# Kernel tuning notes

Hardware: AMD Instinct MI355X
Metric: run time of the kernel (lower is better)

## Reference

```python
import math
import jax, jax.numpy as jnp
import numpy as np

D_MODEL = 1024
NHEAD = 16
HEAD_DIM = D_MODEL // NHEAD
BATCH = 2
SEQ = 2048


def setup_inputs() -> dict:
    key = jax.random.key(0)
    ks = jax.random.split(key, 8)
    data = jax.random.normal(ks[0], (BATCH, SEQ, D_MODEL), dtype=jnp.float32)
    temporal = jax.random.uniform(ks[1], (BATCH, SEQ), dtype=jnp.float32)
    mask = jnp.zeros((SEQ, SEQ), dtype=jnp.float32)
    s = 1.0 / math.sqrt(D_MODEL)
    Wq = jax.random.normal(ks[2], (D_MODEL, D_MODEL), dtype=jnp.float32) * s
    Wk = jax.random.normal(ks[3], (D_MODEL, D_MODEL), dtype=jnp.float32) * s
    Wv = jax.random.normal(ks[4], (D_MODEL, D_MODEL), dtype=jnp.float32) * s
    bq = jax.random.normal(ks[5], (D_MODEL,), dtype=jnp.float32) * 0.02
    bk = jax.random.normal(ks[6], (D_MODEL,), dtype=jnp.float32) * 0.02
    bv = jax.random.normal(ks[7], (D_MODEL,), dtype=jnp.float32) * 0.02
    return {"data": data, "temporal": temporal, "mask": mask,
            "Wq": Wq, "bq": bq, "Wk": Wk, "bk": bk, "Wv": Wv, "bv": bv}


def _rotate_half_pairs(x):
    # x: [..., s] with s even; pairs (x0,x1) -> (-x1, x0) interleaved
    x2 = x.reshape(x.shape[:-1] + (-1, 2))  # [..., s//2, 2]
    rot = jnp.stack([-x2[..., 1], x2[..., 0]], axis=-1)
    return rot.reshape(x.shape)


def reference(data, temporal, mask, Wq, bq, Wk, bk, Wv, bv):
    B, L, D = data.shape
    H, S = NHEAD, HEAD_DIM
    scale = math.sqrt(S)

    query = (data @ Wq + bq).reshape(B, L, H, S)
    key_ = (data @ Wk + bk).reshape(B, L, H, S)
    value = (data @ Wv + bv).reshape(B, L, H, S)

    # freq = 10000^(-arange(0, S, 2)/S), repeat_interleave(2) -> [S]
    freq = jnp.power(10000.0, -jnp.arange(0, S, 2, dtype=jnp.float32) / S)
    freq = jnp.repeat(freq, 2)
    freqs = temporal[:, :, None] * freq[None, None, :]  # [B, L, S]
    cosine = jnp.cos(freqs)[:, :, None, :]  # [B, L, 1, S]
    sine = jnp.sin(freqs)[:, :, None, :]

    rq = query * cosine + _rotate_half_pairs(query) * sine
    rk = key_ * cosine + _rotate_half_pairs(key_) * sine

    logits = jnp.einsum('bqhs,bkhs->bhqk', rq, rk) / scale
    logits = logits + mask  # mask: [L, L], broadcasts over b,h
    weights = jax.nn.softmax(logits, axis=-1)
    context = jnp.einsum('bhqk,bkhs->bqhs', weights, value)
    return context.reshape(B, L, D)
```

## Files before the change

kernel.cpp:

```cpp
#include <hip/hip_runtime.h>
#include <hip/hip_bf16.h>

#define D_MODEL 1024
#define NHEAD   16
#define HEAD_DIM 64
#define BATCH   2
#define SEQ     2048
#define NTOK    (BATCH*SEQ)

#define FREQ_LOG2 0.20762050593046015f

typedef short  bfrag __attribute__((ext_vector_type(8)));
typedef float  ffrag __attribute__((ext_vector_type(4)));

__device__ inline ushort f2bf(float x) {
    __hip_bfloat16 h = __float2bfloat16(x);
    return __builtin_bit_cast(ushort, h);
}
__device__ inline float bf2f(ushort u) {
    return __builtin_bit_cast(float, (uint)u << 16);
}
__device__ inline void split_bf(float x, ushort& hi, ushort& lo) {
    __hip_bfloat16 h = __float2bfloat16(x);
    hi = __builtin_bit_cast(ushort, h);
    lo = f2bf(x - __bfloat162float(h));
}

__device__ inline void gload16(const ushort* g, ushort* l) {
    __builtin_amdgcn_global_load_lds(
        (const __attribute__((address_space(1))) void*)g,
        (__attribute__((address_space(3))) void*)l, 16, 0, 0);
}

__device__ inline void barrier_lds_only() {
    asm volatile("s_waitcnt lgkmcnt(0)\n\ts_barrier" ::: "memory");
}

__device__ inline void barrier_vm4() {
    asm volatile("s_waitcnt vmcnt(4) lgkmcnt(0)\n\ts_barrier" ::: "memory");
}

__device__ inline void barrier_vm8() {
    asm volatile("s_waitcnt vmcnt(8) lgkmcnt(0)\n\ts_barrier" ::: "memory");
}

__global__ __launch_bounds__(256)
void prep(const float* __restrict__ data, ushort* __restrict__ Ahi,
          ushort* __restrict__ Alo,
          const float* __restrict__ mask, ushort* __restrict__ Mbf,
          int* __restrict__ MZnz,
          const float* __restrict__ Wq, const float* __restrict__ Wk,
          const float* __restrict__ Wv, ushort* __restrict__ WThi,
          const float* __restrict__ temporal, float* __restrict__ cst)
{
    __shared__ float T[64][65];
    __shared__ int bnz;
    const int bid = blockIdx.x, t = threadIdx.x;

    if (bid < 4096) {
        const int i4 = (bid * 256 + t) * 4;
        const float4 v = *(const float4*)(data + i4);
        ushort4 h, l;
        split_bf(v.x, h.x, l.x); split_bf(v.y, h.y, l.y);
        split_bf(v.z, h.z, l.z); split_bf(v.w, h.w, l.w);
        *(ushort4*)(Ahi + i4) = h;
        *(ushort4*)(Alo + i4) = l;
        return;
    }
    if (bid < 8192) {
        const int mi = bid - 4096;
        const int i4 = (mi * 256 + t) * 4;
        const float4 v = *(const float4*)(mask + i4);
        ushort4 h;
        h.x = f2bf(v.x); h.y = f2bf(v.y); h.z = f2bf(v.z); h.w = f2bf(v.w);
        *(ushort4*)(Mbf + i4) = h;
        const int nz = (v.x != 0.f) || (v.y != 0.f) || (v.z != 0.f) || (v.w != 0.f);
        if (t == 0) bnz = 0;
        __syncthreads();
        if (nz) atomicOr(&bnz, 1);
        __syncthreads();
        if (t == 0) MZnz[mi] = bnz;
        return;
    }
    if (bid < 8960) {
        const int id  = bid - 8192;
        const int z   = id >> 8;
        const int rem = id & 255;
        const int k0  = (rem & 15) * 64, n0 = (rem >> 4) * 64;
        const float* W = (z == 0) ? Wq : (z == 1) ? Wk : Wv;
        ushort* thi = WThi + (size_t)z * D_MODEL * D_MODEL;

        #pragma unroll
        for (int i = 0; i < 4; i++) {
            const int f = i * 256 + t, r = f >> 4, c = (f & 15) * 4;
            const float4 v = *(const float4*)(W + (size_t)(k0 + r) * D_MODEL + n0 + c);
            T[r][c] = v.x; T[r][c + 1] = v.y; T[r][c + 2] = v.z; T[r][c + 3] = v.w;
        }
        __syncthreads();
        #pragma unroll
        for (int i = 0; i < 4; i++) {
            const int f = i * 256 + t, nr = f >> 4, kc = (f & 15) * 4;
            ushort4 h;
            h.x = f2bf(T[kc + 0][nr]);
            h.y = f2bf(T[kc + 1][nr]);
            h.z = f2bf(T[kc + 2][nr]);
            h.w = f2bf(T[kc + 3][nr]);
            const size_t o = (size_t)(n0 + nr) * D_MODEL + k0 + kc;
            *(ushort4*)(thi + o) = h;
        }
        return;
    }
    const int id3 = bid - 8960;
    const int m   = id3 * 8 + (t >> 5);
    const int j   = t & 31;
    const float tv = temporal[m];
    const float fr = exp2f(-(float)(2 * j) * FREQ_LOG2);
    float s, c;
    __sincosf(tv * fr, &s, &c);
    *(float2*)(cst + (size_t)m * 64 + 2 * j) = make_float2(c, s);
}

#define BK 32

union GemmSM {
    ushort st[3][2][128 * BK];
    float  c[64 * 132];
};

__global__ __launch_bounds__(256, 3)
void gemm_qkv(const ushort* __restrict__ Ahi, const ushort* __restrict__ Alo,
              const ushort* __restrict__ WThi,
              const float* __restrict__ bq, const float* __restrict__ bk,
              const float* __restrict__ bv, const float* __restrict__ cst,
              const int* __restrict__ MZnz, int* __restrict__ Flag,
              ushort* __restrict__ Qhi, ushort* __restrict__ Qlo,
              ushort* __restrict__ Khi,
              ushort* __restrict__ VT)
{
    __shared__ GemmSM sm;
    __shared__ int flg;
    const int bidl = blockIdx.x;
    const int xcd  = bidl & 7, kk = bidl >> 3;
    const int m0   = (xcd * 4 + (kk & 3)) * 128;
    const int nz   = kk >> 2;
    const int n0   = (nz & 7) * 128;
    const int z    = nz >> 3;

    const int t = threadIdx.x;

    if (bidl == 0) {
        if (t == 0) flg = 0;
        __syncthreads();
        int acc = 0;
        const int4* z4 = (const int4*)MZnz;
        #pragma unroll
        for (int i = 0; i < 4; i++) {
            const int4 v = z4[t * 4 + i];
            acc |= v.x | v.y | v.z | v.w;
        }
        if (acc) atomicOr(&flg, 1);
        __syncthreads();
        if (t == 0) Flag[0] = flg;
    }

    const float* bias = (z == 0) ? bq : (z == 1) ? bk : bv;
    const ushort* Bh = WThi + (size_t)z * D_MODEL * D_MODEL;

    const int w = t >> 6, lane = t & 63;
    const int lane15 = lane & 15, quad8 = (lane >> 4) * 8, quad = lane >> 4;
    const int wm = (w >> 1) * 64, wn = (w & 1) * 64;

    ffrag acc[4][4];
    #pragma unroll
    for (int i = 0; i < 4; i++)
        #pragma unroll
        for (int j = 0; j < 4; j++) acc[i][j] = (ffrag){0.f, 0.f, 0.f, 0.f};

    const int wr = w * 32;
    const int lr = lane >> 2;
    const int lc = (((lane & 3) ^ ((lane >> 3) & 3))) * 8;

    auto stage = [&](int bsel, int k0) {
        #pragma unroll
        for (int ch = 0; ch < 2; ch++) {
            const int rb = wr + ch * 16;
            const ushort* ga = Ahi + (size_t)(m0 + rb + lr) * D_MODEL + k0 + lc;
            const ushort* gb = Bh  + (size_t)(n0 + rb + lr) * D_MODEL + k0 + lc;
            gload16(ga, &sm.st[bsel][0][rb * BK]);
            gload16(gb, &sm.st[bsel][1][rb * BK]);
        }
    };

    bfrag alp0, alp1, alp2, alp3;
    {
        alp0 = *(const bfrag*)(Alo + (size_t)(m0 + wm +  0 + lane15) * D_MODEL + quad8);
        alp1 = *(const bfrag*)(Alo + (size_t)(m0 + wm + 16 + lane15) * D_MODEL + quad8);
        alp2 = *(const bfrag*)(Alo + (size_t)(m0 + wm + 32 + lane15) * D_MODEL + quad8);
        alp3 = *(const bfrag*)(Alo + (size_t)(m0 + wm + 48 + lane15) * D_MODEL + quad8);
    }

    stage(0, 0);
    stage(1, BK);
    barrier_vm4();

    const int rdsw = (quad ^ ((lane15 >> 1) & 3)) * 8;

    int cur = 0;
    for (int i = 0; i < 32; i++) {
        const int k0 = i * BK;
        const int st2 = (cur >= 1) ? cur - 1 : 2;
        stage(st2, k0 + 2 * BK);

        bfrag al0 = alp0, al1 = alp1, al2 = alp2, al3 = alp3;
        {
            const int kn = k0 + BK;
            alp0 = *(const bfrag*)(Alo + (size_t)(m0 + wm +  0 + lane15) * D_MODEL + kn + quad8);
            alp1 = *(const bfrag*)(Alo + (size_t)(m0 + wm + 16 + lane15) * D_MODEL + kn + quad8);
            alp2 = *(const bfrag*)(Alo + (size_t)(m0 + wm + 32 + lane15) * D_MODEL + kn + quad8);
            alp3 = *(const bfrag*)(Alo + (size_t)(m0 + wm + 48 + lane15) * D_MODEL + kn + quad8);
        }

        bfrag ah[4];
        #pragma unroll
        for (int mt = 0; mt < 4; mt++)
            ah[mt] = *(const bfrag*)&sm.st[cur][0][(wm + mt * 16 + lane15) * BK + rdsw];

        #pragma unroll
        for (int nt = 0; nt < 4; nt++) {
            const bfrag bh = *(const bfrag*)&sm.st[cur][1][(wn + nt * 16 + lane15) * BK + rdsw];
            {
                ffrag a = acc[0][nt];
                a = __builtin_amdgcn_mfma_f32_16x16x32_bf16(ah[0], bh, a, 0, 0, 0);
                a = __builtin_amdgcn_mfma_f32_16x16x32_bf16(al0,   bh, a, 0, 0, 0);
                acc[0][nt] = a;
            }
            {
                ffrag a = acc[1][nt];
                a = __builtin_amdgcn_mfma_f32_16x16x32_bf16(ah[1], bh, a, 0, 0, 0);
                a = __builtin_amdgcn_mfma_f32_16x16x32_bf16(al1,   bh, a, 0, 0, 0);
                acc[1][nt] = a;
            }
            {
                ffrag a = acc[2][nt];
                a = __builtin_amdgcn_mfma_f32_16x16x32_bf16(ah[2], bh, a, 0, 0, 0);
                a = __builtin_amdgcn_mfma_f32_16x16x32_bf16(al2,   bh, a, 0, 0, 0);
                acc[2][nt] = a;
            }
            {
                ffrag a = acc[3][nt];
                a = __builtin_amdgcn_mfma_f32_16x16x32_bf16(ah[3], bh, a, 0, 0, 0);
                a = __builtin_amdgcn_mfma_f32_16x16x32_bf16(al3,   bh, a, 0, 0, 0);
                acc[3][nt] = a;
            }
        }
        barrier_vm8();
        cur = (cur == 2) ? 0 : cur + 1;
    }

    float bn[4];
    #pragma unroll
    for (int nt = 0; nt < 4; nt++) bn[nt] = bias[n0 + wn + nt * 16 + lane15];

    const int CST = (z == 2) ? 129 : 132;

    #pragma unroll
    for (int p = 0; p < 2; p++) {
        if (p) __syncthreads();
        if ((w >> 1) == p) {
            #pragma unroll
            for (int mt = 0; mt < 4; mt++)
                #pragma unroll
                for (int nt = 0; nt < 4; nt++)
                    #pragma unroll
                    for (int rr = 0; rr < 4; rr++)
                        sm.c[(mt * 16 + quad * 4 + rr) * CST + wn + nt * 16 + lane15] =
                            acc[mt][nt][rr] + bn[nt];
        }
        __syncthreads();

        if (z < 2) {
            ushort* ohi = (z == 0) ? Qhi : Khi;
            const float sc = (z == 0) ? 0.125f : 1.0f;
            #pragma unroll
            for (int i = 0; i < 8; i++) {
                const int f = i * 256 + t, r = f >> 5, c4 = (f & 31) * 4;
                float4 v = *(float4*)&sm.c[r * 132 + c4];
                const int m = m0 + p * 64 + r;
                const float4 cs4 = *(const float4*)(cst + (size_t)m * 64 + (c4 & 63));
                const float c0 = cs4.x, s0 = cs4.y, c1v = cs4.z, s1 = cs4.w;
                const float y0 = (v.x * c0 - v.y * s0) * sc;
                const float y1 = (v.y * c0 + v.x * s0) * sc;
                const float y2 = (v.z * c1v - v.w * s1) * sc;
                const float y3 = (v.w * c1v + v.z * s1) * sc;
                ushort4 h, l;
                split_bf(y0, h.x, l.x); split_bf(y1, h.y, l.y);
                split_bf(y2, h.z, l.z); split_bf(y3, h.w, l.w);
                const size_t o = (size_t)m * D_MODEL + n0 + c4;
                *(ushort4*)(ohi + o) = h;
                if (z == 0) *(ushort4*)(Qlo + o) = l;
            }
        } else {
            const int bb = m0 >> 11;
            #pragma unroll
            for (int i = 0; i < 4; i++) {
                const int cid = i * 256 + t, col = cid >> 3, tg = (cid & 7) * 8;
                ushort u8[8];
                #pragma unroll
                for (int j = 0; j < 8; j++) u8[j] = f2bf(sm.c[(tg + j) * 129 + col]);
                const int ncol = n0 + col, hh = ncol >> 6, d = ncol & 63;
                const size_t dst = ((size_t)(bb * NHEAD + hh) * HEAD_DIM + d) * SEQ +
                                   (m0 & (SEQ - 1)) + p * 64 + tg;
                *(int4*)(VT + dst) = *(int4*)u8;
            }
        }
    }
}

__global__ __launch_bounds__(256, 2)
void attn_mfma(const ushort* __restrict__ Qhi, const ushort* __restrict__ Qlo,
               const ushort* __restrict__ Khi,
               const ushort* __restrict__ VT,  const ushort* __restrict__ maskbf,
               const int* __restrict__ Flag,
               float* __restrict__ out)
{
    __shared__ ushort lsK[2][64 * 64], lsV[2][64 * 64], lsP[128 * 64];

    const int bid  = blockIdx.x;
    const int bh   = (bid & 7) * 4 + (bid >> 7);
    const int qb   = (bid >> 3) & 15;
    const int b    = bh >> 4, h = bh & 15;
    const int q0   = qb * 128;

    const int t = threadIdx.x, w = t >> 6, lane = t & 63;
    const int lane15 = lane & 15, quad = lane >> 4;
    const size_t tok0 = (size_t)b * SEQ;

    const int mz = Flag[0];

    bfrag qh[2][2], ql[2][2];
    #pragma unroll
    for (int su = 0; su < 2; su++) {
        const size_t qrow = (tok0 + q0 + w * 32 + su * 16 + lane15) * D_MODEL +
                            h * HEAD_DIM;
        #pragma unroll
        for (int ks = 0; ks < 2; ks++) {
            qh[su][ks] = *(const bfrag*)(Qhi + qrow + ks * 32 + quad * 8);
            ql[su][ks] = *(const bfrag*)(Qlo + qrow + ks * 32 + quad * 8);
        }
    }

    ffrag of[2][4];
    float l_i[2][4];
    #pragma unroll
    for (int su = 0; su < 2; su++)
        #pragma unroll
        for (int nt = 0; nt < 4; nt++) {
            of[su][nt] = (ffrag){0.f, 0.f, 0.f, 0.f};
            l_i[su][nt] = 0.f;
        }

    const int r1 = t >> 3,  c1 = (t & 7) * 8;
    const int sw = ((t & 7) ^ (r1 & 7)) * 8;
    const ushort* Kh0 = Khi + tok0 * D_MODEL + h * HEAD_DIM;
    const ushort* Vt0 = VT + (size_t)(b * NHEAD + h) * HEAD_DIM * SEQ;

    int4 pk0 = *(const int4*)(Kh0 + (size_t)r1 * D_MODEL + c1);
    int4 pk1 = *(const int4*)(Kh0 + (size_t)(32 + r1) * D_MODEL + c1);
    int4 pv0 = *(const int4*)(Vt0 + (size_t)r1 * SEQ + c1);
    int4 pv1 = *(const int4*)(Vt0 + (size_t)(32 + r1) * SEQ + c1);

    *(int4*)&lsK[0][r1 * 64 + sw]        = pk0;
    *(int4*)&lsK[0][(32 + r1) * 64 + sw] = pk1;
    *(int4*)&lsV[0][r1 * 64 + sw]        = pv0;
    *(int4*)&lsV[0][(32 + r1) * 64 + sw] = pv1;

    pk0 = *(const int4*)(Kh0 + (size_t)(64 + r1) * D_MODEL + c1);
    pk1 = *(const int4*)(Kh0 + (size_t)(96 + r1) * D_MODEL + c1);
    pv0 = *(const int4*)(Vt0 + (size_t)r1 * SEQ + 64 + c1);
    pv1 = *(const int4*)(Vt0 + (size_t)(32 + r1) * SEQ + 64 + c1);
    barrier_lds_only();

    const ushort* mrow0 = maskbf + (size_t)(q0 + w * 32 + quad * 4) * SEQ;
    const ushort* mrow1 = maskbf + (size_t)(q0 + w * 32 + 16 + quad * 4) * SEQ;

    const int krd  = lane15 & 7;
    const int keyr = (((lane15 >> 2) & 3) << 1) | (lane15 & 1);

    int cur = 0;
    for (int kt = 0; kt < SEQ; kt += 64) {
        if (kt + 64 < SEQ) {
            *(int4*)&lsK[cur ^ 1][r1 * 64 + sw]        = pk0;
            *(int4*)&lsK[cur ^ 1][(32 + r1) * 64 + sw] = pk1;
            *(int4*)&lsV[cur ^ 1][r1 * 64 + sw]        = pv0;
            *(int4*)&lsV[cur ^ 1][(32 + r1) * 64 + sw] = pv1;
        }

        float mv0[4][4], mv1[4][4];
        if (mz) {
            #pragma unroll
            for (int nt = 0; nt < 4; nt++)
                #pragma unroll
                for (int rr = 0; rr < 4; rr++) {
                    mv0[nt][rr] = bf2f(mrow0[(size_t)rr * SEQ + kt + nt * 16 + lane15]);
                    mv1[nt][rr] = bf2f(mrow1[(size_t)rr * SEQ + kt + nt * 16 + lane15]);
                }
        }

        const int ktn = (kt + 128 < SEQ) ? kt + 128 : 0;
        pk0 = *(const int4*)(Kh0 + (size_t)(ktn + r1) * D_MODEL + c1);
        pk1 = *(const int4*)(Kh0 + (size_t)(ktn + 32 + r1) * D_MODEL + c1);
        pv0 = *(const int4*)(Vt0 + (size_t)r1 * SEQ + ktn + c1);
        pv1 = *(const int4*)(Vt0 + (size_t)(32 + r1) * SEQ + ktn + c1);

        ffrag s0[4], s1[4];
        __builtin_amdgcn_s_setprio(1);
        #pragma unroll
        for (int nt = 0; nt < 4; nt++) {
            const bfrag kf0 = *(const bfrag*)&lsK[cur][(nt * 16 + lane15) * 64 +
                                                       ((0 + quad) ^ krd) * 8];
            const bfrag kf1 = *(const bfrag*)&lsK[cur][(nt * 16 + lane15) * 64 +
                                                       ((4 + quad) ^ krd) * 8];
            ffrag a0 = (ffrag){0.f, 0.f, 0.f, 0.f};
            ffrag a1 = (ffrag){0.f, 0.f, 0.f, 0.f};
            a0 = __builtin_amdgcn_mfma_f32_16x16x32_bf16(qh[0][0], kf0, a0, 0, 0, 0);
            a0 = __builtin_amdgcn_mfma_f32_16x16x32_bf16(ql[0][0], kf0, a0, 0, 0, 0);
            a0 = __builtin_amdgcn_mfma_f32_16x16x32_bf16(qh[0][1], kf1, a0, 0, 0, 0);
            a0 = __builtin_amdgcn_mfma_f32_16x16x32_bf16(ql[0][1], kf1, a0, 0, 0, 0);
            a1 = __builtin_amdgcn_mfma_f32_16x16x32_bf16(qh[1][0], kf0, a1, 0, 0, 0);
            a1 = __builtin_amdgcn_mfma_f32_16x16x32_bf16(ql[1][0], kf0, a1, 0, 0, 0);
            a1 = __builtin_amdgcn_mfma_f32_16x16x32_bf16(qh[1][1], kf1, a1, 0, 0, 0);
            a1 = __builtin_amdgcn_mfma_f32_16x16x32_bf16(ql[1][1], kf1, a1, 0, 0, 0);
            s0[nt] = a0;
            s1[nt] = a1;
        }
        __builtin_amdgcn_s_setprio(0);

        #pragma unroll
        for (int nt = 0; nt < 4; nt++)
            #pragma unroll
            for (int rr = 0; rr < 4; rr++) {
                const int pchk = (2 * nt + (lane15 >> 3)) ^ ((quad << 1) | (rr & 1));
                float x0 = s0[nt][rr];
                float x1 = s1[nt][rr];
                if (mz) { x0 += mv0[nt][rr]; x1 += mv1[nt][rr]; }
                const float e0 = __expf(x0);
                l_i[0][rr] += e0;
                lsP[(w * 32 + quad * 4 + rr) * 64 + pchk * 8 + (lane15 & 7)] = f2bf(e0);
                const float e1 = __expf(x1);
                l_i[1][rr] += e1;
                lsP[(w * 32 + 16 + quad * 4 + rr) * 64 + pchk * 8 + (lane15 & 7)] = f2bf(e1);
            }

        __builtin_amdgcn_s_setprio(1);
        #pragma unroll
        for (int ks = 0; ks < 2; ks++) {
            const bfrag pf0 = *(const bfrag*)&lsP[(w * 32 + lane15) * 64 +
                                                  ((ks * 4 + quad) ^ keyr) * 8];
            const bfrag pf1 = *(const bfrag*)&lsP[(w * 32 + 16 + lane15) * 64 +
                                                  ((ks * 4 + quad) ^ keyr) * 8];
            #pragma unroll
            for (int nt = 0; nt < 4; nt++) {
                const bfrag vf = *(const bfrag*)&lsV[cur][(nt * 16 + lane15) * 64 +
                                                          ((ks * 4 + quad) ^ krd) * 8];
                of[0][nt] = __builtin_amdgcn_mfma_f32_16x16x32_bf16(pf0, vf, of[0][nt], 0, 0, 0);
                of[1][nt] = __builtin_amdgcn_mfma_f32_16x16x32_bf16(pf1, vf, of[1][nt], 0, 0, 0);
            }
        }
        __builtin_amdgcn_s_setprio(0);

        barrier_lds_only();
        cur ^= 1;
    }

    #pragma unroll
    for (int su = 0; su < 2; su++) {
        float inv[4];
        #pragma unroll
        for (int rr = 0; rr < 4; rr++) {
            float v = l_i[su][rr];
            #pragma unroll
            for (int off = 1; off < 16; off <<= 1) v += __shfl_xor(v, off);
            inv[rr] = 1.0f / v;
        }
        #pragma unroll
        for (int nt = 0; nt < 4; nt++)
            #pragma unroll
            for (int rr = 0; rr < 4; rr++)
                out[(tok0 + q0 + w * 32 + su * 16 + quad * 4 + rr) * D_MODEL +
                    h * HEAD_DIM + nt * 16 + lane15] = of[su][nt][rr] * inv[rr];
    }
}

extern "C" void kernel_launch(void* const* d_in, const int* in_sizes, int n_in,
                              void* d_out, int out_size, void* d_ws, size_t ws_size,
                              hipStream_t stream)
{
    const float* data     = (const float*)d_in[0];
    const float* temporal = (const float*)d_in[1];
    const float* mask     = (const float*)d_in[2];
    const float* Wq = (const float*)d_in[3];
    const float* bq = (const float*)d_in[4];
    const float* Wk = (const float*)d_in[5];
    const float* bk = (const float*)d_in[6];
    const float* Wv = (const float*)d_in[7];
    const float* bv = (const float*)d_in[8];
    float* out = (float*)d_out;

    char* ws = (char*)d_ws;
    const size_t MB = 1024 * 1024;
    ushort* Ahi  = (ushort*)(ws + 0 * MB);
    ushort* Alo  = (ushort*)(ws + 8 * MB);
    ushort* WThi = (ushort*)(ws + 16 * MB);
    int*    MZnz = (int*)   (ws + 22 * MB);
    int*    Flag = (int*)   (ws + 23 * MB);
    float*  cst  = (float*) (ws + 24 * MB);
    ushort* Qhi  = (ushort*)(ws + 28 * MB);
    ushort* Qlo  = (ushort*)(ws + 36 * MB);
    ushort* Khi  = (ushort*)(ws + 44 * MB);
    ushort* VT   = (ushort*)(ws + 60 * MB);
    ushort* Mbf  = (ushort*)(ws + 68 * MB);

    prep<<<dim3(9472), 256, 0, stream>>>(data, Ahi, Alo, mask, Mbf, MZnz,
                                         Wq, Wk, Wv, WThi, temporal, cst);
    gemm_qkv<<<dim3(768), 256, 0, stream>>>(
        Ahi, Alo, WThi, bq, bk, bv, cst, MZnz, Flag,
        Qhi, Qlo, Khi, VT);
    attn_mfma<<<dim3(BATCH * NHEAD * SEQ / 128), 256, 0, stream>>>(
        Qhi, Qlo, Khi, VT, Mbf, Flag, out);
}
```

Measured before the change: 239.7 us.

## Double the K/V tile per pipeline stage to 128 keys with new V swizzle

The attention loop now stages 128 keys of K and V per double-buffered step and processes them as two 64-key halves, so it needs half as many block barriers and prefetch rounds. The V tile layout is widened to 128 columns per row with a new XOR swizzle to avoid LDS bank conflicts. In exchange, LDS usage rises (about 80KB per block with two blocks per CU) and each thread holds more prefetch registers, which could limit occupancy. The lsP tile written in the second half reuses the buffer without an intervening barrier, which relies on per-wave row ownership.

Result: faster. 234.6 us (-2.1%).

```diff
diff --git a/kernel.cpp b/kernel.cpp
--- a/kernel.cpp
+++ b/kernel.cpp
@@ -323,7 +323,7 @@
                const int* __restrict__ Flag,
                float* __restrict__ out)
 {
-    __shared__ ushort lsK[2][64 * 64], lsV[2][64 * 64], lsP[128 * 64];
+    __shared__ ushort lsK[2][128 * 64], lsV[2][64 * 128], lsP[128 * 64];
 
     const int bid  = blockIdx.x;
     const int bh   = (bid & 7) * 4 + (bid >> 7);
@@ -359,25 +359,39 @@
             l_i[su][nt] = 0.f;
         }
 
-    const int r1 = t >> 3,  c1 = (t & 7) * 8;
-    const int sw = ((t & 7) ^ (r1 & 7)) * 8;
+    const int rK  = t >> 3, cK = (t & 7) * 8;
+    const int swK = ((t & 7) ^ (rK & 7)) * 8;
+    const int rV   = t >> 2;
+    const int keyV = ((rV & 3) << 2) | ((rV >> 2) & 3);
     const ushort* Kh0 = Khi + tok0 * D_MODEL + h * HEAD_DIM;
     const ushort* Vt0 = VT + (size_t)(b * NHEAD + h) * HEAD_DIM * SEQ;
 
-    int4 pk0 = *(const int4*)(Kh0 + (size_t)r1 * D_MODEL + c1);
-    int4 pk1 = *(const int4*)(Kh0 + (size_t)(32 + r1) * D_MODEL + c1);
-    int4 pv0 = *(const int4*)(Vt0 + (size_t)r1 * SEQ + c1);
-    int4 pv1 = *(const int4*)(Vt0 + (size_t)(32 + r1) * SEQ + c1);
-
-    *(int4*)&lsK[0][r1 * 64 + sw]        = pk0;
-    *(int4*)&lsK[0][(32 + r1) * 64 + sw] = pk1;
-    *(int4*)&lsV[0][r1 * 64 + sw]        = pv0;
-    *(int4*)&lsV[0][(32 + r1) * 64 + sw] = pv1;
-
-    pk0 = *(const int4*)(Kh0 + (size_t)(64 + r1) * D_MODEL + c1);
-    pk1 = *(const int4*)(Kh0 + (size_t)(96 + r1) * D_MODEL + c1);
-    pv0 = *(const int4*)(Vt0 + (size_t)r1 * SEQ + 64 + c1);
-    pv1 = *(const int4*)(Vt0 + (size_t)(32 + r1) * SEQ + 64 + c1);
+    int4 pk0 = *(const int4*)(Kh0 + (size_t)(rK +  0) * D_MODEL + cK);
+    int4 pk1 = *(const int4*)(Kh0 + (size_t)(rK + 32) * D_MODEL + cK);
+    int4 pk2 = *(const int4*)(Kh0 + (size_t)(rK + 64) * D_MODEL + cK);
+    int4 pk3 = *(const int4*)(Kh0 + (size_t)(rK + 96) * D_MODEL + cK);
+    int4 pv0 = *(const int4*)(Vt0 + (size_t)rV * SEQ + (t & 3) * 8 +  0);
+    int4 pv1 = *(const int4*)(Vt0 + (size_t)rV * SEQ + (t & 3) * 8 + 32);
+    int4 pv2 = *(const int4*)(Vt0 + (size_t)rV * SEQ + (t & 3) * 8 + 64);
+    int4 pv3 = *(const int4*)(Vt0 + (size_t)rV * SEQ + (t & 3) * 8 + 96);
+
+    *(int4*)&lsK[0][(rK +  0) * 64 + swK] = pk0;
+    *(int4*)&lsK[0][(rK + 32) * 64 + swK] = pk1;
+    *(int4*)&lsK[0][(rK + 64) * 64 + swK] = pk2;
+    *(int4*)&lsK[0][(rK + 96) * 64 + swK] = pk3;
+    *(int4*)&lsV[0][rV * 128 + (((t & 3) +  0) ^ keyV) * 8] = pv0;
+    *(int4*)&lsV[0][rV * 128 + (((t & 3) +  4) ^ keyV) * 8] = pv1;
+    *(int4*)&lsV[0][rV * 128 + (((t & 3) +  8) ^ keyV) * 8] = pv2;
+    *(int4*)&lsV[0][rV * 128 + (((t & 3) + 12) ^ keyV) * 8] = pv3;
+
+    pk0 = *(const int4*)(Kh0 + (size_t)(128 + rK +  0) * D_MODEL + cK);
+    pk1 = *(const int4*)(Kh0 + (size_t)(128 + rK + 32) * D_MODEL + cK);
+    pk2 = *(const int4*)(Kh0 + (size_t)(128 + rK + 64) * D_MODEL + cK);
+    pk3 = *(const int4*)(Kh0 + (size_t)(128 + rK + 96) * D_MODEL + cK);
+    pv0 = *(const int4*)(Vt0 + (size_t)rV * SEQ + 128 + (t & 3) * 8 +  0);
+    pv1 = *(const int4*)(Vt0 + (size_t)rV * SEQ + 128 + (t & 3) * 8 + 32);
+    pv2 = *(const int4*)(Vt0 + (size_t)rV * SEQ + 128 + (t & 3) * 8 + 64);
+    pv3 = *(const int4*)(Vt0 + (size_t)rV * SEQ + 128 + (t & 3) * 8 + 96);
     barrier_lds_only();
 
     const ushort* mrow0 = maskbf + (size_t)(q0 + w * 32 + quad * 4) * SEQ;
@@ -385,88 +399,102 @@
 
     const int krd  = lane15 & 7;
     const int keyr = (((lane15 >> 2) & 3) << 1) | (lane15 & 1);
+    const int keyVr = ((lane15 & 3) << 2) | ((lane15 >> 2) & 3);
 
     int cur = 0;
-    for (int kt = 0; kt < SEQ; kt += 64) {
-        if (kt + 64 < SEQ) {
-            *(int4*)&lsK[cur ^ 1][r1 * 64 + sw]        = pk0;
-            *(int4*)&lsK[cur ^ 1][(32 + r1) * 64 + sw] = pk1;
-            *(int4*)&lsV[cur ^ 1][r1 * 64 + sw]        = pv0;
-            *(int4*)&lsV[cur ^ 1][(32 + r1) * 64 + sw] = pv1;
-        }
-
-        float mv0[4][4], mv1[4][4];
-        if (mz) {
+    for (int kt = 0; kt < SEQ; kt += 128) {
+        if (kt + 128 < SEQ) {
+            *(int4*)&lsK[cur ^ 1][(rK +  0) * 64 + swK] = pk0;
+            *(int4*)&lsK[cur ^ 1][(rK + 32) * 64 + swK] = pk1;
+            *(int4*)&lsK[cur ^ 1][(rK + 64) * 64 + swK] = pk2;
+            *(int4*)&lsK[cur ^ 1][(rK + 96) * 64 + swK] = pk3;
+            *(int4*)&lsV[cur ^ 1][rV * 128 + (((t & 3) +  0) ^ keyV) * 8] = pv0;
+            *(int4*)&lsV[cur ^ 1][rV * 128 + (((t & 3) +  4) ^ keyV) * 8] = pv1;
+            *(int4*)&lsV[cur ^ 1][rV * 128 + (((t & 3) +  8) ^ keyV) * 8] = pv2;
+            *(int4*)&lsV[cur ^ 1][rV * 128 + (((t & 3) + 12) ^ keyV) * 8] = pv3;
+        }
+
+        const int ktn = (kt + 256 < SEQ) ? kt + 256 : 0;
+        pk0 = *(const int4*)(Kh0 + (size_t)(ktn + rK +  0) * D_MODEL + cK);
+        pk1 = *(const int4*)(Kh0 + (size_t)(ktn + rK + 32) * D_MODEL + cK);
+        pk2 = *(const int4*)(Kh0 + (size_t)(ktn + rK + 64) * D_MODEL + cK);
+        pk3 = *(const int4*)(Kh0 + (size_t)(ktn + rK + 96) * D_MODEL + cK);
+        pv0 = *(const int4*)(Vt0 + (size_t)rV * SEQ + ktn + (t & 3) * 8 +  0);
+        pv1 = *(const int4*)(Vt0 + (size_t)rV * SEQ + ktn + (t & 3) * 8 + 32);
+        pv2 = *(const int4*)(Vt0 + (size_t)rV * SEQ + ktn + (t & 3) * 8 + 64);
+        pv3 = *(const int4*)(Vt0 + (size_t)rV * SEQ + ktn + (t & 3) * 8 + 96);
+
+        #pragma unroll
+        for (int half = 0; half < 2; half++) {
+            const int kb = kt + half * 64;
+
+            float mv0[4][4], mv1[4][4];
+            if (mz) {
+                #pragma unroll
+                for (int nt = 0; nt < 4; nt++)
+                    #pragma unroll
+                    for (int rr = 0; rr < 4; rr++) {
+                        mv0[nt][rr] = bf2f(mrow0[(size_t)rr * SEQ + kb + nt * 16 + lane15]);
+                        mv1[nt][rr] = bf2f(mrow1[(size_t)rr * SEQ + kb + nt * 16 + lane15]);
+                    }
+            }
+
+            ffrag s0[4], s1[4];
+            __builtin_amdgcn_s_setprio(1);
+            #pragma unroll
+            for (int nt = 0; nt < 4; nt++) {
+                const int krow = half * 64 + nt * 16 + lane15;
+                const bfrag kf0 = *(const bfrag*)&lsK[cur][krow * 64 + ((0 + quad) ^ krd) * 8];
+                const bfrag kf1 = *(const bfrag*)&lsK[cur][krow * 64 + ((4 + quad) ^ krd) * 8];
+                ffrag a0 = (ffrag){0.f, 0.f, 0.f, 0.f};
+                ffrag a1 = (ffrag){0.f, 0.f, 0.f, 0.f};
+                a0 = __builtin_amdgcn_mfma_f32_16x16x32_bf16(qh[0][0], kf0, a0, 0, 0, 0);
+                a0 = __builtin_amdgcn_mfma_f32_16x16x32_bf16(ql[0][0], kf0, a0, 0, 0, 0);
+                a0 = __builtin_amdgcn_mfma_f32_16x16x32_bf16(qh[0][1], kf1, a0, 0, 0, 0);
+                a0 = __builtin_amdgcn_mfma_f32_16x16x32_bf16(ql[0][1], kf1, a0, 0, 0, 0);
+                a1 = __builtin_amdgcn_mfma_f32_16x16x32_bf16(qh[1][0], kf0, a1, 0, 0, 0);
+                a1 = __builtin_amdgcn_mfma_f32_16x16x32_bf16(ql[1][0], kf0, a1, 0, 0, 0);
+                a1 = __builtin_amdgcn_mfma_f32_16x16x32_bf16(qh[1][1], kf1, a1, 0, 0, 0);
+                a1 = __builtin_amdgcn_mfma_f32_16x16x32_bf16(ql[1][1], kf1, a1, 0, 0, 0);
+                s0[nt] = a0;
+                s1[nt] = a1;
+            }
+            __builtin_amdgcn_s_setprio(0);
+
             #pragma unroll
             for (int nt = 0; nt < 4; nt++)
                 #pragma unroll
                 for (int rr = 0; rr < 4; rr++) {
-                    mv0[nt][rr] = bf2f(mrow0[(size_t)rr * SEQ + kt + nt * 16 + lane15]);
-                    mv1[nt][rr] = bf2f(mrow1[(size_t)rr * SEQ + kt + nt * 16 + lane15]);
+                    const int pchk = (2 * nt + (lane15 >> 3)) ^ ((quad << 1) | (rr & 1));
+                    float x0 = s0[nt][rr];
+                    float x1 = s1[nt][rr];
+                    if (mz) { x0 += mv0[nt][rr]; x1 += mv1[nt][rr]; }
+                    const float e0 = __expf(x0);
+                    l_i[0][rr] += e0;
+                    lsP[(w * 32 + quad * 4 + rr) * 64 + pchk * 8 + (lane15 & 7)] = f2bf(e0);
+                    const float e1 = __expf(x1);
+                    l_i[1][rr] += e1;
+                    lsP[(w * 32 + 16 + quad * 4 + rr) * 64 + pchk * 8 + (lane15 & 7)] = f2bf(e1);
                 }
-        }
-
-        const int ktn = (kt + 128 < SEQ) ? kt + 128 : 0;
-        pk0 = *(const int4*)(Kh0 + (size_t)(ktn + r1) * D_MODEL + c1);
-        pk1 = *(const int4*)(Kh0 + (size_t)(ktn + 32 + r1) * D_MODEL + c1);
-        pv0 = *(const int4*)(Vt0 + (size_t)r1 * SEQ + ktn + c1);
-        pv1 = *(const int4*)(Vt0 + (size_t)(32 + r1) * SEQ + ktn + c1);
-
-        ffrag s0[4], s1[4];
-        __builtin_amdgcn_s_setprio(1);
-        #pragma unroll
-        for (int nt = 0; nt < 4; nt++) {
-            const bfrag kf0 = *(const bfrag*)&lsK[cur][(nt * 16 + lane15) * 64 +
-                                                       ((0 + quad) ^ krd) * 8];
-            const bfrag kf1 = *(const bfrag*)&lsK[cur][(nt * 16 + lane15) * 64 +
-                                                       ((4 + quad) ^ krd) * 8];
-            ffrag a0 = (ffrag){0.f, 0.f, 0.f, 0.f};
-            ffrag a1 = (ffrag){0.f, 0.f, 0.f, 0.f};
-            a0 = __builtin_amdgcn_mfma_f32_16x16x32_bf16(qh[0][0], kf0, a0, 0, 0, 0);
-            a0 = __builtin_amdgcn_mfma_f32_16x16x32_bf16(ql[0][0], kf0, a0, 0, 0, 0);
-            a0 = __builtin_amdgcn_mfma_f32_16x16x32_bf16(qh[0][1], kf1, a0, 0, 0, 0);
-            a0 = __builtin_amdgcn_mfma_f32_16x16x32_bf16(ql[0][1], kf1, a0, 0, 0, 0);
-            a1 = __builtin_amdgcn_mfma_f32_16x16x32_bf16(qh[1][0], kf0, a1, 0, 0, 0);
-            a1 = __builtin_amdgcn_mfma_f32_16x16x32_bf16(ql[1][0], kf0, a1, 0, 0, 0);
-            a1 = __builtin_amdgcn_mfma_f32_16x16x32_bf16(qh[1][1], kf1, a1, 0, 0, 0);
-            a1 = __builtin_amdgcn_mfma_f32_16x16x32_bf16(ql[1][1], kf1, a1, 0, 0, 0);
-            s0[nt] = a0;
-            s1[nt] = a1;
-        }
-        __builtin_amdgcn_s_setprio(0);
-
-        #pragma unroll
-        for (int nt = 0; nt < 4; nt++)
-            #pragma unroll
-            for (int rr = 0; rr < 4; rr++) {
-                const int pchk = (2 * nt + (lane15 >> 3)) ^ ((quad << 1) | (rr & 1));
-                float x0 = s0[nt][rr];
-                float x1 = s1[nt][rr];
-                if (mz) { x0 += mv0[nt][rr]; x1 += mv1[nt][rr]; }
-                const float e0 = __expf(x0);
-                l_i[0][rr] += e0;
-                lsP[(w * 32 + quad * 4 + rr) * 64 + pchk * 8 + (lane15 & 7)] = f2bf(e0);
-                const float e1 = __expf(x1);
-                l_i[1][rr] += e1;
-                lsP[(w * 32 + 16 + quad * 4 + rr) * 64 + pchk * 8 + (lane15 & 7)] = f2bf(e1);
-            }
-
-        __builtin_amdgcn_s_setprio(1);
-        #pragma unroll
-        for (int ks = 0; ks < 2; ks++) {
-            const bfrag pf0 = *(const bfrag*)&lsP[(w * 32 + lane15) * 64 +
-                                                  ((ks * 4 + quad) ^ keyr) * 8];
-            const bfrag pf1 = *(const bfrag*)&lsP[(w * 32 + 16 + lane15) * 64 +
-                                                  ((ks * 4 + quad) ^ keyr) * 8];
-            #pragma unroll
-            for (int nt = 0; nt < 4; nt++) {
-                const bfrag vf = *(const bfrag*)&lsV[cur][(nt * 16 + lane15) * 64 +
-                                                          ((ks * 4 + quad) ^ krd) * 8];
-                of[0][nt] = __builtin_amdgcn_mfma_f32_16x16x32_bf16(pf0, vf, of[0][nt], 0, 0, 0);
-                of[1][nt] = __builtin_amdgcn_mfma_f32_16x16x32_bf16(pf1, vf, of[1][nt], 0, 0, 0);
-            }
-        }
-        __builtin_amdgcn_s_setprio(0);
+
+            __builtin_amdgcn_s_setprio(1);
+            #pragma unroll
+            for (int ksl = 0; ksl < 2; ksl++) {
+                const bfrag pf0 = *(const bfrag*)&lsP[(w * 32 + lane15) * 64 +
+                                                      ((ksl * 4 + quad) ^ keyr) * 8];
+                const bfrag pf1 = *(const bfrag*)&lsP[(w * 32 + 16 + lane15) * 64 +
+                                                      ((ksl * 4 + quad) ^ keyr) * 8];
+                const int lkc = half * 8 + ksl * 4 + quad;
+                #pragma unroll
+                for (int nt = 0; nt < 4; nt++) {
+                    const bfrag vf = *(const bfrag*)&lsV[cur][(nt * 16 + lane15) * 128 +
+                                                              (lkc ^ keyVr) * 8];
+                    of[0][nt] = __builtin_amdgcn_mfma_f32_16x16x32_bf16(pf0, vf, of[0][nt], 0, 0, 0);
+                    of[1][nt] = __builtin_amdgcn_mfma_f32_16x16x32_bf16(pf1, vf, of[1][nt], 0, 0, 0);
+                }
+            }
+            __builtin_amdgcn_s_setprio(0);
+        }
 
         barrier_lds_only();
         cur ^= 1;
```
